# Optimization experiments

Measured on AMD Instinct MI355X. Metric: run time of the kernel, lower is better.

The kernel has to match this reference:

```python
import jax, jax.numpy as jnp
import numpy as np
import math

B, S, D, H = 2, 2048, 1024, 16
DK = D // H


def setup_inputs() -> dict:
    key = jax.random.key(0)
    ks = jax.random.split(key, 12)
    std = 1.0 / math.sqrt(D)
    inp = {
        "query": jax.random.normal(ks[0], (B, S, D), jnp.float32),
        "key": jax.random.normal(ks[1], (B, S, D), jnp.float32),
        "value": jax.random.normal(ks[2], (B, S, D), jnp.float32),
        # causal mask, broadcast over batch and heads
        "mask": jnp.tril(jnp.ones((S, S), jnp.int32))[None, None, :, :],
        # nn.Linear weights are [out_features, in_features]
        "Wq": jax.random.uniform(ks[3], (D, D), jnp.float32, -std, std),
        "bq": jax.random.uniform(ks[4], (D,), jnp.float32, -std, std),
        "Wk": jax.random.uniform(ks[5], (D, D), jnp.float32, -std, std),
        "bk": jax.random.uniform(ks[6], (D,), jnp.float32, -std, std),
        "Wv": jax.random.uniform(ks[7], (D, D), jnp.float32, -std, std),
        "bv": jax.random.uniform(ks[8], (D,), jnp.float32, -std, std),
        "Wo": jax.random.uniform(ks[9], (D, D), jnp.float32, -std, std),
        "bo": jax.random.uniform(ks[10], (D,), jnp.float32, -std, std),
    }
    return inp


def reference(query, key, value, mask, Wq, bq, Wk, bk, Wv, bv, Wo, bo):
    q = query @ Wq.T + bq  # [B,S,D]
    k = key @ Wk.T + bk
    v = value @ Wv.T + bv
    # Faithful to the original: a raw view (reshape), NOT a head-transpose split.
    q = q.reshape(B, H, S, DK)
    k = k.reshape(B, H, S, DK)
    v = v.reshape(B, H, S, DK)
    scores = jnp.einsum("bhqd,bhkd->bhqk", q, k) / math.sqrt(DK)
    scores = jnp.where(mask == 0, jnp.float32(-1e9), scores)
    weights = jax.nn.softmax(scores, axis=-1)
    # dropout(p=0.1) is identity in eval mode
    context = jnp.einsum("bhqk,bhkd->bhqd", weights, v)
    context = context.transpose(0, 2, 1, 3).reshape(B, S, D)
    return context @ Wo.T + bo
```

## Files before the change

### kernel.cpp

```cpp
#include <hip/hip_runtime.h>
#include <hip/hip_bf16.h>

#define BB 2
#define SS 2048
#define DD 1024
#define HH 16
#define DKK 64

typedef __attribute__((ext_vector_type(4))) float  f32x4;
typedef __attribute__((ext_vector_type(8))) short  s16x8;
typedef __attribute__((ext_vector_type(4))) short  s16x4;
typedef __attribute__((ext_vector_type(4))) float  fvec4;
typedef __attribute__((ext_vector_type(2))) unsigned int u32x2;

__device__ __forceinline__ short f2bs(float f) {
    union { __hip_bfloat16 b; short s; } u;
    u.b = __float2bfloat16(f);
    return u.s;
}

__device__ __forceinline__ unsigned cvtpk(float lo, float hi) {
    unsigned r;
    asm("v_cvt_pk_bf16_f32 %0, %1, %2" : "=v"(r) : "v"(lo), "v"(hi));
    return r;
}

__device__ __forceinline__ void gload_lds16(const short* g, short* l) {
    __builtin_amdgcn_global_load_lds((const __attribute__((address_space(1))) void*)g,
                                     (__attribute__((address_space(3))) void*)l, 16, 0, 0);
}

__global__ __launch_bounds__(256) void cvt_all(
    const float* __restrict__ q,  const float* __restrict__ k,  const float* __restrict__ v,
    const float* __restrict__ wq, const float* __restrict__ wk, const float* __restrict__ wv,
    const float* __restrict__ wo,
    short* __restrict__ qo,  short* __restrict__ ko,  short* __restrict__ vo,
    short* __restrict__ wqo, short* __restrict__ wko, short* __restrict__ wvo,
    short* __restrict__ woo)
{
    const float* src; short* dst; int n;
    switch (blockIdx.y) {
        case 0: src = q;  dst = qo;  n = BB * SS * DD; break;
        case 1: src = k;  dst = ko;  n = BB * SS * DD; break;
        case 2: src = v;  dst = vo;  n = BB * SS * DD; break;
        case 3: src = wq; dst = wqo; n = DD * DD; break;
        case 4: src = wk; dst = wko; n = DD * DD; break;
        case 5: src = wv; dst = wvo; n = DD * DD; break;
        default: src = wo; dst = woo; n = DD * DD; break;
    }
    int i = (blockIdx.x * 256 + threadIdx.x) * 8;
    const int stride = gridDim.x * 256 * 8;
    for (; i < n; i += stride) {
        fvec4 a = *(const fvec4*)&src[i];
        fvec4 b = *(const fvec4*)&src[i + 4];
        s16x8 o;
        o[0] = f2bs(a[0]); o[1] = f2bs(a[1]); o[2] = f2bs(a[2]); o[3] = f2bs(a[3]);
        o[4] = f2bs(b[0]); o[5] = f2bs(b[1]); o[6] = f2bs(b[2]); o[7] = f2bs(b[3]);
        *(s16x8*)&dst[i] = o;
    }
}

template<int BN, int NXSH, bool OUTF32>
__global__ __launch_bounds__(256) void gemm_nt_v2(
    const short* __restrict__ A0, const short* __restrict__ A1, const short* __restrict__ A2,
    const short* __restrict__ B0, const short* __restrict__ B1, const short* __restrict__ B2,
    const float* __restrict__ c0, const float* __restrict__ c1, const float* __restrict__ c2,
    void* __restrict__ O0, void* __restrict__ O1, void* __restrict__ O2,
    float os0, float os1, float os2,
    int ppx, int NY, int KL, int N, int K)
{
    const int d   = blockIdx.x;
    const int xcd = d & 7;
    const int s   = d >> 3;
    const int x   = s & ((1 << NXSH) - 1);
    const int pl  = s >> NXSH;
    const int panel = xcd * ppx + pl;
    const int y   = panel % NY;
    const int z   = panel / NY;

    const short* A    = z == 0 ? A0 : (z == 1 ? A1 : A2);
    const short* Bw   = z == 0 ? B0 : (z == 1 ? B1 : B2);
    const float* bias = z == 0 ? c0 : (z == 1 ? c1 : c2);
    void* Cp          = z == 0 ? O0 : (z == 1 ? O1 : O2);
    const float oscale = z == 0 ? os0 : (z == 1 ? os1 : os2);

    __shared__ short As[128][64];
    __shared__ short Bs[BN][64];

    const int tid  = threadIdx.x;
    const int lane = tid & 63;
    const int wid  = tid >> 6;
    const int r16  = lane & 15;
    const int g    = lane >> 4;
    const int m0   = y * 128;
    const int n0   = x * BN;
    constexpr int MR = 4;
    constexpr int NR = BN / 32;
    const int wr   = (wid >> 1) * 64;
    const int wc   = (wid & 1) * (BN / 2);
    const int srow8 = lane >> 3;
    const int c8    = lane & 7;

    f32x4 acc[MR][NR];
#pragma unroll
    for (int mi = 0; mi < MR; ++mi)
#pragma unroll
        for (int ni = 0; ni < NR; ++ni) acc[mi][ni] = (f32x4){0.f, 0.f, 0.f, 0.f};

    const int csrc = (c8 ^ srow8) * 8;
    const int nk = KL >> 6;
#pragma unroll 1
    for (int kt = 0; kt < nk; ++kt) {
        const int k0 = kt * 64;
        if (kt) __syncthreads();
#pragma unroll
        for (int q = 0; q < 4; ++q) {
            const int r = wid * 32 + q * 8 + srow8;
            gload_lds16(&A[(size_t)(m0 + r) * K + k0 + csrc], &As[wid * 32 + q * 8][0]);
        }
#pragma unroll
        for (int q = 0; q < BN / 32; ++q) {
            const int r = wid * (BN / 4) + q * 8 + srow8;
            gload_lds16(&Bw[(size_t)(n0 + r) * K + k0 + csrc], &Bs[wid * (BN / 4) + q * 8][0]);
        }
        __syncthreads();

#pragma unroll
        for (int kk = 0; kk < 2; ++kk) {
            s16x8 af[MR], bf[NR];
#pragma unroll
            for (int mi = 0; mi < MR; ++mi) {
                const int row = wr + mi * 16 + r16;
                af[mi] = *(const s16x8*)&As[row][((kk * 4 + g) ^ (row & 7)) * 8];
            }
#pragma unroll
            for (int ni = 0; ni < NR; ++ni) {
                const int row = wc + ni * 16 + r16;
                bf[ni] = *(const s16x8*)&Bs[row][((kk * 4 + g) ^ (row & 7)) * 8];
            }
#pragma unroll
            for (int mi = 0; mi < MR; ++mi)
#pragma unroll
                for (int ni = 0; ni < NR; ++ni)
                    acc[mi][ni] = __builtin_amdgcn_mfma_f32_16x16x32_bf16(
                        bf[ni], af[mi], acc[mi][ni], 0, 0, 0);
        }
    }

#pragma unroll
    for (int mi = 0; mi < MR; ++mi) {
        const size_t row = (size_t)(m0 + wr + mi * 16 + r16);
#pragma unroll
        for (int ni = 0; ni < NR; ++ni) {
            const int colb = n0 + wc + ni * 16 + g * 4;
            fvec4 bv;
            if (bias) bv = *(const fvec4*)&bias[colb];
            else      bv = (fvec4){0.f, 0.f, 0.f, 0.f};
            const f32x4 a = acc[mi][ni];
            const float v0 = (a[0] + bv[0]) * oscale;
            const float v1 = (a[1] + bv[1]) * oscale;
            const float v2 = (a[2] + bv[2]) * oscale;
            const float v3 = (a[3] + bv[3]) * oscale;
            if constexpr (OUTF32) {
                fvec4 o; o[0] = v0; o[1] = v1; o[2] = v2; o[3] = v3;
                *(fvec4*)&((float*)Cp)[row * N + colb] = o;
            } else {
                u32x2 w;
                w[0] = cvtpk(v0, v1);
                w[1] = cvtpk(v2, v3);
                *(u32x2*)&((short*)Cp)[row * N + colb] = w;
            }
        }
    }
}

__global__ __launch_bounds__(256) void mha_transpose_v(
    const short* __restrict__ vp, short* __restrict__ vT)
{
    const int st = blockIdx.x;
    const int bh = blockIdx.y;
    const short* src = vp + (size_t)bh * SS * DKK;
    short*       dst = vT + (size_t)bh * SS * DKK;
    const int tid = threadIdx.x;
#pragma unroll
    for (int i = 0; i < 2; ++i) {
        const int c  = tid + i * 256;
        const int dk = c >> 3;
        const int sc = c & 7;
        const int s0 = st * 64 + sc * 8;
        s16x8 v;
#pragma unroll
        for (int j = 0; j < 8; ++j) v[j] = src[(size_t)(s0 + j) * DKK + dk];
        *(s16x8*)&dst[(size_t)dk * SS + s0] = v;
    }
}

__global__ __launch_bounds__(256, 2) void mha_attn(
    const short* __restrict__ qp, const short* __restrict__ kp,
    const short* __restrict__ vT, short* __restrict__ ctx)
{
    __shared__ short Ks[64][64];
    __shared__ short Vs[64][64];
    __shared__ short P[4][16][72];

    const int tid  = threadIdx.x;
    const int wid  = tid >> 6;
    const int lane = tid & 63;
    const int r16  = lane & 15;
    const int g    = lane >> 4;

    const int bh  = blockIdx.x;
    const int bxp = blockIdx.y;
    const int b   = bh >> 4;
    const int h   = bh & 15;

    const short* Qh = qp + (size_t)bh * SS * DKK;
    const short* Kh = kp + (size_t)bh * SS * DKK;
    const short* Vh = vT + (size_t)bh * SS * DKK;

    const int srow = lane >> 3;
    const int csw  = (((lane & 7) ^ srow) & 7) * 8;
    const int r0   = wid * 16;

#pragma unroll 1
    for (int t = 0; t < 2; ++t) {
        const int grp = t ? (31 - bxp) : bxp;
        const int qr0 = grp * 64 + wid * 16;
        const int nkt = grp + 1;

        const s16x8 qf0 = *(const s16x8*)&Qh[(size_t)(qr0 + r16) * DKK + g * 8];
        const s16x8 qf1 = *(const s16x8*)&Qh[(size_t)(qr0 + r16) * DKK + 32 + g * 8];

        f32x4 po[4];
#pragma unroll
        for (int i = 0; i < 4; ++i) po[i] = (f32x4){0.f, 0.f, 0.f, 0.f};
        float lsum = 0.f;

#pragma unroll 1
        for (int j = 0; j < nkt; ++j) {
            const int k0 = j * 64;
            __syncthreads();
            {
                const int rowA = r0 + srow;
                const int rowB = rowA + 8;
                gload_lds16(&Kh[(size_t)(k0 + rowA) * DKK + csw], &Ks[r0][0]);
                gload_lds16(&Kh[(size_t)(k0 + rowB) * DKK + csw], &Ks[r0 + 8][0]);
                gload_lds16(&Vh[(size_t)rowA * SS + k0 + csw], &Vs[r0][0]);
                gload_lds16(&Vh[(size_t)rowB * SS + k0 + csw], &Vs[r0 + 8][0]);
            }
            __syncthreads();

            f32x4 sc[4];
            __builtin_amdgcn_s_setprio(1);
#pragma unroll
            for (int cg = 0; cg < 4; ++cg) {
                const int R  = cg * 16 + r16;
                const int sw = R & 7;
                const s16x8 kf0 = *(const s16x8*)&Ks[R][((g ^ sw) & 7) * 8];
                const s16x8 kf1 = *(const s16x8*)&Ks[R][(((4 + g) ^ sw) & 7) * 8];
                f32x4 tt = (f32x4){0.f, 0.f, 0.f, 0.f};
                tt = __builtin_amdgcn_mfma_f32_16x16x32_bf16(kf0, qf0, tt, 0, 0, 0);
                tt = __builtin_amdgcn_mfma_f32_16x16x32_bf16(kf1, qf1, tt, 0, 0, 0);
                sc[cg] = tt;
            }
            __builtin_amdgcn_s_setprio(0);

            if (j == nkt - 1) {
#pragma unroll
                for (int cg = 0; cg < 4; ++cg)
#pragma unroll
                    for (int r = 0; r < 4; ++r)
                        if (k0 + cg * 16 + g * 4 + r > qr0 + r16) sc[cg][r] = -1e9f;
            }
#pragma unroll
            for (int cg = 0; cg < 4; ++cg) {
                const float p0 = __expf(sc[cg][0]);
                const float p1 = __expf(sc[cg][1]);
                const float p2 = __expf(sc[cg][2]);
                const float p3 = __expf(sc[cg][3]);
                lsum += (p0 + p1) + (p2 + p3);
                u32x2 w;
                w[0] = cvtpk(p0, p1);
                w[1] = cvtpk(p2, p3);
                *(u32x2*)&P[wid][r16][cg * 16 + g * 4] = w;
            }
            const s16x8 pf0 = *(const s16x8*)&P[wid][r16][g * 8];
            const s16x8 pf1 = *(const s16x8*)&P[wid][r16][32 + g * 8];

            __builtin_amdgcn_s_setprio(1);
#pragma unroll
            for (int dg = 0; dg < 4; ++dg) {
                const int Rv = dg * 16 + r16;
                const int sw = Rv & 7;
                const s16x8 vf0 = *(const s16x8*)&Vs[Rv][((g ^ sw) & 7) * 8];
                const s16x8 vf1 = *(const s16x8*)&Vs[Rv][(((4 + g) ^ sw) & 7) * 8];
                po[dg] = __builtin_amdgcn_mfma_f32_16x16x32_bf16(pf0, vf0, po[dg], 0, 0, 0);
                po[dg] = __builtin_amdgcn_mfma_f32_16x16x32_bf16(pf1, vf1, po[dg], 0, 0, 0);
            }
            __builtin_amdgcn_s_setprio(0);
        }

        lsum += __shfl_xor(lsum, 16);
        lsum += __shfl_xor(lsum, 32);
        const float linv = __builtin_amdgcn_rcpf(lsum);
        float rowinv[4];
#pragma unroll
        for (int r = 0; r < 4; ++r)
            rowinv[r] = __shfl(linv, g * 4 + r);
#pragma unroll
        for (int dg = 0; dg < 4; ++dg)
#pragma unroll
            for (int r = 0; r < 4; ++r) {
                const int srw = qr0 + g * 4 + r;
                const float v = po[dg][r] * rowinv[r];
                ctx[((size_t)(b * SS + srw)) * DD + h * 64 + dg * 16 + r16] = f2bs(v);
            }
    }
}

extern "C" void kernel_launch(void* const* d_in, const int* in_sizes, int n_in,
                              void* d_out, int out_size, void* d_ws, size_t ws_size,
                              hipStream_t stream) {
    const float* query = (const float*)d_in[0];
    const float* key   = (const float*)d_in[1];
    const float* value = (const float*)d_in[2];
    const float* Wq = (const float*)d_in[4];
    const float* bq = (const float*)d_in[5];
    const float* Wk = (const float*)d_in[6];
    const float* bk = (const float*)d_in[7];
    const float* Wv = (const float*)d_in[8];
    const float* bv = (const float*)d_in[9];
    const float* Wo = (const float*)d_in[10];
    const float* bo = (const float*)d_in[11];
    float* out = (float*)d_out;

    const size_t elems = (size_t)BB * SS * DD;
    const size_t wel   = (size_t)DD * DD;
    short* qx  = (short*)d_ws;
    short* kx  = qx + elems;
    short* vx  = kx + elems;
    short* wqx = vx + elems;
    short* wkx = wqx + wel;
    short* wvx = wkx + wel;
    short* wox = wvx + wel;
    short* qp  = wox + wel;
    short* kp  = qp + elems;
    short* vp  = kp + elems;
    short* vT  = qx;
    short* ctx = vx;

    cvt_all<<<dim3(1024, 7), 256, 0, stream>>>(query, key, value, Wq, Wk, Wv, Wo,
                                               qx, kx, vx, wqx, wkx, wvx, wox);
    gemm_nt_v2<128, 3, false><<<dim3(768), 256, 0, stream>>>(
        qx, kx, vx, wqx, wkx, wvx, bq, bk, bv, qp, kp, vp,
        0.125f, 1.0f, 1.0f, 12, 32, 1024, DD, DD);
    mha_transpose_v<<<dim3(SS / 64, BB * HH), 256, 0, stream>>>(vp, vT);
    mha_attn<<<dim3(BB * HH, 16), 256, 0, stream>>>(qp, kp, vT, ctx);
    gemm_nt_v2<64, 4, true><<<dim3(512), 256, 0, stream>>>(
        ctx, ctx, ctx, wox, wox, wox, bo, bo, bo, out, out, out,
        1.0f, 1.0f, 1.0f, 4, 32, 1024, DD, DD);
}
```

Before: 124.0 us.

## Fuse V transpose into QKV GEMM epilogue and flatten attention grid

The V projection epilogue now writes its output directly in the transposed per-head layout the attention kernel consumes. This removes the separate transpose kernel launch and its extra read and write of V. The attention kernel also drops its two-pass loop that paired light and heavy causal row groups. It now launches one block per query group, 1024 blocks in total, with an XCD-aware mapping and a remapped group order meant to balance work. The trade-off is that the transposed V stores are scattered 2-byte writes with stride SS, which may coalesce poorly, and each block now does unequal work.

```diff
diff --git a/kernel.cpp b/kernel.cpp
--- a/kernel.cpp
+++ b/kernel.cpp
@@ -67,7 +67,7 @@
     const float* __restrict__ c0, const float* __restrict__ c1, const float* __restrict__ c2,
     void* __restrict__ O0, void* __restrict__ O1, void* __restrict__ O2,
     float os0, float os1, float os2,
-    int ppx, int NY, int KL, int N, int K)
+    int ppx, int NY, int KL, int N, int K, int vtmode)
 {
     const int d   = blockIdx.x;
     const int xcd = d & 7;
@@ -147,6 +147,7 @@
         }
     }
 
+    const bool vt = (vtmode != 0) && (z == 2);
 #pragma unroll
     for (int mi = 0; mi < MR; ++mi) {
         const size_t row = (size_t)(m0 + wr + mi * 16 + r16);
@@ -165,33 +166,23 @@
                 fvec4 o; o[0] = v0; o[1] = v1; o[2] = v2; o[3] = v3;
                 *(fvec4*)&((float*)Cp)[row * N + colb] = o;
             } else {
-                u32x2 w;
-                w[0] = cvtpk(v0, v1);
-                w[1] = cvtpk(v2, v3);
-                *(u32x2*)&((short*)Cp)[row * N + colb] = w;
+                if (vt) {
+                    const int bhh = (int)(row >> 7);
+                    const int sW  = ((int)row & 127) * 16 + (colb >> 6);
+                    short* dst = (short*)Cp + (size_t)bhh * SS * DKK
+                               + (size_t)(colb & 63) * SS + sW;
+                    dst[0 * SS] = f2bs(v0);
+                    dst[1 * SS] = f2bs(v1);
+                    dst[2 * SS] = f2bs(v2);
+                    dst[3 * SS] = f2bs(v3);
+                } else {
+                    u32x2 w;
+                    w[0] = cvtpk(v0, v1);
+                    w[1] = cvtpk(v2, v3);
+                    *(u32x2*)&((short*)Cp)[row * N + colb] = w;
+                }
             }
         }
-    }
-}
-
-__global__ __launch_bounds__(256) void mha_transpose_v(
-    const short* __restrict__ vp, short* __restrict__ vT)
-{
-    const int st = blockIdx.x;
-    const int bh = blockIdx.y;
-    const short* src = vp + (size_t)bh * SS * DKK;
-    short*       dst = vT + (size_t)bh * SS * DKK;
-    const int tid = threadIdx.x;
-#pragma unroll
-    for (int i = 0; i < 2; ++i) {
-        const int c  = tid + i * 256;
-        const int dk = c >> 3;
-        const int sc = c & 7;
-        const int s0 = st * 64 + sc * 8;
-        s16x8 v;
-#pragma unroll
-        for (int j = 0; j < 8; ++j) v[j] = src[(size_t)(s0 + j) * DKK + dk];
-        *(s16x8*)&dst[(size_t)dk * SS + s0] = v;
     }
 }
 
@@ -209,8 +200,12 @@
     const int r16  = lane & 15;
     const int g    = lane >> 4;
 
-    const int bh  = blockIdx.x;
-    const int bxp = blockIdx.y;
+    const int lin = blockIdx.x;
+    const int xcd = lin & 7;
+    const int s8  = lin >> 3;
+    const int bh  = (xcd << 2) | (s8 & 3);
+    const int v   = s8 >> 2;
+    const int grp = (v < 16) ? v : (47 - v);
     const int b   = bh >> 4;
     const int h   = bh & 15;
 
@@ -222,100 +217,96 @@
     const int csw  = (((lane & 7) ^ srow) & 7) * 8;
     const int r0   = wid * 16;
 
+    const int qr0 = grp * 64 + wid * 16;
+    const int nkt = grp + 1;
+
+    const s16x8 qf0 = *(const s16x8*)&Qh[(size_t)(qr0 + r16) * DKK + g * 8];
+    const s16x8 qf1 = *(const s16x8*)&Qh[(size_t)(qr0 + r16) * DKK + 32 + g * 8];
+
+    f32x4 po[4];
+#pragma unroll
+    for (int i = 0; i < 4; ++i) po[i] = (f32x4){0.f, 0.f, 0.f, 0.f};
+    float lsum = 0.f;
+
 #pragma unroll 1
-    for (int t = 0; t < 2; ++t) {
-        const int grp = t ? (31 - bxp) : bxp;
-        const int qr0 = grp * 64 + wid * 16;
-        const int nkt = grp + 1;
-
-        const s16x8 qf0 = *(const s16x8*)&Qh[(size_t)(qr0 + r16) * DKK + g * 8];
-        const s16x8 qf1 = *(const s16x8*)&Qh[(size_t)(qr0 + r16) * DKK + 32 + g * 8];
-
-        f32x4 po[4];
-#pragma unroll
-        for (int i = 0; i < 4; ++i) po[i] = (f32x4){0.f, 0.f, 0.f, 0.f};
-        float lsum = 0.f;
-
-#pragma unroll 1
-        for (int j = 0; j < nkt; ++j) {
-            const int k0 = j * 64;
-            __syncthreads();
-            {
-                const int rowA = r0 + srow;
-                const int rowB = rowA + 8;
-                gload_lds16(&Kh[(size_t)(k0 + rowA) * DKK + csw], &Ks[r0][0]);
-                gload_lds16(&Kh[(size_t)(k0 + rowB) * DKK + csw], &Ks[r0 + 8][0]);
-                gload_lds16(&Vh[(size_t)rowA * SS + k0 + csw], &Vs[r0][0]);
-                gload_lds16(&Vh[(size_t)rowB * SS + k0 + csw], &Vs[r0 + 8][0]);
-            }
-            __syncthreads();
-
-            f32x4 sc[4];
-            __builtin_amdgcn_s_setprio(1);
-#pragma unroll
-            for (int cg = 0; cg < 4; ++cg) {
-                const int R  = cg * 16 + r16;
-                const int sw = R & 7;
-                const s16x8 kf0 = *(const s16x8*)&Ks[R][((g ^ sw) & 7) * 8];
-                const s16x8 kf1 = *(const s16x8*)&Ks[R][(((4 + g) ^ sw) & 7) * 8];
-                f32x4 tt = (f32x4){0.f, 0.f, 0.f, 0.f};
-                tt = __builtin_amdgcn_mfma_f32_16x16x32_bf16(kf0, qf0, tt, 0, 0, 0);
-                tt = __builtin_amdgcn_mfma_f32_16x16x32_bf16(kf1, qf1, tt, 0, 0, 0);
-                sc[cg] = tt;
-            }
-            __builtin_amdgcn_s_setprio(0);
-
-            if (j == nkt - 1) {
-#pragma unroll
-                for (int cg = 0; cg < 4; ++cg)
-#pragma unroll
-                    for (int r = 0; r < 4; ++r)
-                        if (k0 + cg * 16 + g * 4 + r > qr0 + r16) sc[cg][r] = -1e9f;
-            }
-#pragma unroll
-            for (int cg = 0; cg < 4; ++cg) {
-                const float p0 = __expf(sc[cg][0]);
-                const float p1 = __expf(sc[cg][1]);
-                const float p2 = __expf(sc[cg][2]);
-                const float p3 = __expf(sc[cg][3]);
-                lsum += (p0 + p1) + (p2 + p3);
-                u32x2 w;
-                w[0] = cvtpk(p0, p1);
-                w[1] = cvtpk(p2, p3);
-                *(u32x2*)&P[wid][r16][cg * 16 + g * 4] = w;
-            }
-            const s16x8 pf0 = *(const s16x8*)&P[wid][r16][g * 8];
-            const s16x8 pf1 = *(const s16x8*)&P[wid][r16][32 + g * 8];
-
-            __builtin_amdgcn_s_setprio(1);
-#pragma unroll
-            for (int dg = 0; dg < 4; ++dg) {
-                const int Rv = dg * 16 + r16;
-                const int sw = Rv & 7;
-                const s16x8 vf0 = *(const s16x8*)&Vs[Rv][((g ^ sw) & 7) * 8];
-                const s16x8 vf1 = *(const s16x8*)&Vs[Rv][(((4 + g) ^ sw) & 7) * 8];
-                po[dg] = __builtin_amdgcn_mfma_f32_16x16x32_bf16(pf0, vf0, po[dg], 0, 0, 0);
-                po[dg] = __builtin_amdgcn_mfma_f32_16x16x32_bf16(pf1, vf1, po[dg], 0, 0, 0);
-            }
-            __builtin_amdgcn_s_setprio(0);
-        }
-
-        lsum += __shfl_xor(lsum, 16);
-        lsum += __shfl_xor(lsum, 32);
-        const float linv = __builtin_amdgcn_rcpf(lsum);
-        float rowinv[4];
-#pragma unroll
-        for (int r = 0; r < 4; ++r)
-            rowinv[r] = __shfl(linv, g * 4 + r);
-#pragma unroll
-        for (int dg = 0; dg < 4; ++dg)
-#pragma unroll
-            for (int r = 0; r < 4; ++r) {
-                const int srw = qr0 + g * 4 + r;
-                const float v = po[dg][r] * rowinv[r];
-                ctx[((size_t)(b * SS + srw)) * DD + h * 64 + dg * 16 + r16] = f2bs(v);
-            }
-    }
+    for (int j = 0; j < nkt; ++j) {
+        const int k0 = j * 64;
+        __syncthreads();
+        {
+            const int rowA = r0 + srow;
+            const int rowB = rowA + 8;
+            gload_lds16(&Kh[(size_t)(k0 + rowA) * DKK + csw], &Ks[r0][0]);
+            gload_lds16(&Kh[(size_t)(k0 + rowB) * DKK + csw], &Ks[r0 + 8][0]);
+            gload_lds16(&Vh[(size_t)rowA * SS + k0 + csw], &Vs[r0][0]);
+            gload_lds16(&Vh[(size_t)rowB * SS + k0 + csw], &Vs[r0 + 8][0]);
+        }
+        __syncthreads();
+
+        f32x4 sc[4];
+        __builtin_amdgcn_s_setprio(1);
+#pragma unroll
+        for (int cg = 0; cg < 4; ++cg) {
+            const int R  = cg * 16 + r16;
+            const int sw = R & 7;
+            const s16x8 kf0 = *(const s16x8*)&Ks[R][((g ^ sw) & 7) * 8];
+            const s16x8 kf1 = *(const s16x8*)&Ks[R][(((4 + g) ^ sw) & 7) * 8];
+            f32x4 tt = (f32x4){0.f, 0.f, 0.f, 0.f};
+            tt = __builtin_amdgcn_mfma_f32_16x16x32_bf16(kf0, qf0, tt, 0, 0, 0);
+            tt = __builtin_amdgcn_mfma_f32_16x16x32_bf16(kf1, qf1, tt, 0, 0, 0);
+            sc[cg] = tt;
+        }
+        __builtin_amdgcn_s_setprio(0);
+
+        if (j == nkt - 1) {
+#pragma unroll
+            for (int cg = 0; cg < 4; ++cg)
+#pragma unroll
+                for (int r = 0; r < 4; ++r)
+                    if (k0 + cg * 16 + g * 4 + r > qr0 + r16) sc[cg][r] = -1e9f;
+        }
+#pragma unroll
+        for (int cg = 0; cg < 4; ++cg) {
+            const float p0 = __expf(sc[cg][0]);
+            const float p1 = __expf(sc[cg][1]);
+            const float p2 = __expf(sc[cg][2]);
+            const float p3 = __expf(sc[cg][3]);
+            lsum += (p0 + p1) + (p2 + p3);
+            u32x2 w;
+            w[0] = cvtpk(p0, p1);
+            w[1] = cvtpk(p2, p3);
+            *(u32x2*)&P[wid][r16][cg * 16 + g * 4] = w;
+        }
+        const s16x8 pf0 = *(const s16x8*)&P[wid][r16][g * 8];
+        const s16x8 pf1 = *(const s16x8*)&P[wid][r16][32 + g * 8];
+
+        __builtin_amdgcn_s_setprio(1);
+#pragma unroll
+        for (int dg = 0; dg < 4; ++dg) {
+            const int Rv = dg * 16 + r16;
+            const int sw = Rv & 7;
+            const s16x8 vf0 = *(const s16x8*)&Vs[Rv][((g ^ sw) & 7) * 8];
+            const s16x8 vf1 = *(const s16x8*)&Vs[Rv][(((4 + g) ^ sw) & 7) * 8];
+            po[dg] = __builtin_amdgcn_mfma_f32_16x16x32_bf16(pf0, vf0, po[dg], 0, 0, 0);
+            po[dg] = __builtin_amdgcn_mfma_f32_16x16x32_bf16(pf1, vf1, po[dg], 0, 0, 0);
+        }
+        __builtin_amdgcn_s_setprio(0);
+    }
+
+    lsum += __shfl_xor(lsum, 16);
+    lsum += __shfl_xor(lsum, 32);
+    const float linv = __builtin_amdgcn_rcpf(lsum);
+    float rowinv[4];
+#pragma unroll
+    for (int r = 0; r < 4; ++r)
+        rowinv[r] = __shfl(linv, g * 4 + r);
+#pragma unroll
+    for (int dg = 0; dg < 4; ++dg)
+#pragma unroll
+        for (int r = 0; r < 4; ++r) {
+            const int srw = qr0 + g * 4 + r;
+            const float vv = po[dg][r] * rowinv[r];
+            ctx[((size_t)(b * SS + srw)) * DD + h * 64 + dg * 16 + r16] = f2bs(vv);
+        }
 }
 
 extern "C" void kernel_launch(void* const* d_in, const int* in_sizes, int n_in,
@@ -346,17 +337,15 @@
     short* qp  = wox + wel;
     short* kp  = qp + elems;
     short* vp  = kp + elems;
-    short* vT  = qx;
     short* ctx = vx;
 
     cvt_all<<<dim3(1024, 7), 256, 0, stream>>>(query, key, value, Wq, Wk, Wv, Wo,
                                                qx, kx, vx, wqx, wkx, wvx, wox);
     gemm_nt_v2<128, 3, false><<<dim3(768), 256, 0, stream>>>(
         qx, kx, vx, wqx, wkx, wvx, bq, bk, bv, qp, kp, vp,
-        0.125f, 1.0f, 1.0f, 12, 32, 1024, DD, DD);
-    mha_transpose_v<<<dim3(SS / 64, BB * HH), 256, 0, stream>>>(vp, vT);
-    mha_attn<<<dim3(BB * HH, 16), 256, 0, stream>>>(qp, kp, vT, ctx);
+        0.125f, 1.0f, 1.0f, 12, 32, 1024, DD, DD, 1);
+    mha_attn<<<dim3(1024), 256, 0, stream>>>(qp, kp, vp, ctx);
     gemm_nt_v2<64, 4, true><<<dim3(512), 256, 0, stream>>>(
         ctx, ctx, ctx, wox, wox, wox, bo, bo, bo, out, out, out,
-        1.0f, 1.0f, 1.0f, 4, 32, 1024, DD, DD);
-}
+        1.0f, 1.0f, 1.0f, 4, 32, 1024, DD, DD, 0);
+}
```

Result: slower. 133.6 us (+7.7%).
